# Kernel tuning notes

Measured on AMD Instinct MI355X. Metric: run time of the kernel, lower is better.

Reference implementation:

```python
import jax, jax.numpy as jnp
import numpy as np


def _largest_component_mask(fg):
    # fg: (B,H,W) bool foreground mask. Returns bool mask of the largest
    # 8-connected component per batch element (skimage.measure.label default
    # connectivity for 2D is 8-connectivity).
    B, H, W = fg.shape
    HW = H * W
    big = jnp.int32(HW)  # sentinel label for background / padding
    idx = jnp.arange(HW, dtype=jnp.int32).reshape(1, H, W)
    l0 = jnp.broadcast_to(idx, (B, H, W))

    def neighbor_min(l):
        lm = jnp.where(fg, l, big)
        p = jnp.pad(lm, ((0, 0), (1, 1), (1, 1)), constant_values=HW)
        m = lm
        for di in (-1, 0, 1):
            for dj in (-1, 0, 1):
                if di == 0 and dj == 0:
                    continue
                m = jnp.minimum(m, p[:, 1 + di:1 + di + H, 1 + dj:1 + dj + W])
        return m

    def body(carry):
        l, _ = carry
        # one step of label propagation (min over 8-neighborhood, fg only)
        l2 = jnp.where(fg, jnp.minimum(l, neighbor_min(l)), l)
        # pointer jumping: l <- l[l]  (labels are in-row linear indices)
        lf = l2.reshape(B, HW)
        l2 = jnp.take_along_axis(lf, lf, axis=1).reshape(B, H, W)
        return l2, jnp.any(l2 != l)

    l, _ = jax.lax.while_loop(lambda c: c[1], body, (l0, jnp.bool_(True)))

    lf = l.reshape(B, HW)
    w = fg.reshape(B, HW).astype(jnp.float32)
    counts = jax.vmap(lambda li, wi: jnp.bincount(li, weights=wi, length=HW))(lf, w)
    largest = jnp.argmax(counts, axis=1).astype(jnp.int32)  # (B,) root label of biggest cc
    return (l == largest[:, None, None]) & fg


def setup_inputs() -> dict:
    key = jax.random.key(0)
    x = jax.random.normal(key, (16, 2, 1024, 1024), dtype=jnp.float32)
    return {"x": x}


def reference(x):
    # binary segmentation = argmax over class dim; background class = 0
    binary = jnp.argmax(x, axis=1)          # (B,H,W) int
    fg = binary > 0
    mask = _largest_component_mask(fg)       # (B,H,W) bool, largest cc only
    return x * mask[:, None, :, :].astype(x.dtype)
```

## Files before the change

### kernel.cpp

```cpp
#include <hip/hip_runtime.h>
#include <stdint.h>

static constexpr int BATCH = 16;
static constexpr int Hh = 1024;
static constexpr int Ww = 1024;
static constexpr int HW = Hh * Ww;
static constexpr int NPIX = BATCH * HW;
static constexpr int TS = 64;
static constexpr int TILES_PER_IMG = (Hh / TS) * (Ww / TS);
static constexpr int NODES = TS * 32;

static constexpr int CHUNK = 1024;
static constexpr int NBLK1 = NPIX / CHUNK;
static constexpr int BLK1_PER_B = HW / CHUNK;


__device__ __forceinline__ int find_root_halve(int* parent, int i) {
    while (true) {
        int p = parent[i];
        if (p == i) return i;
        int gp = parent[p];
        if (gp == p) return p;
        parent[i] = gp;
        i = gp;
    }
}

__device__ __forceinline__ int find_root_ro(const int* parent, int i) {
    int p = parent[i];
    while (p != i) { i = p; p = parent[i]; }
    return i;
}

__device__ __forceinline__ void merge_uf(int* parent, int a, int b) {
    while (true) {
        a = find_root_halve(parent, a);
        b = find_root_halve(parent, b);
        if (a == b) return;
        if (a > b) { int t = a; a = b; b = t; }
        int old = atomicMin(&parent[b], a);
        if (old == b) return;
        b = old;
    }
}


__global__ __launch_bounds__(256) void k_local(const float* __restrict__ x,
                                               int* __restrict__ parent,
                                               int* __restrict__ counts,
                                               unsigned long long* __restrict__ best) {
    __shared__ int lab[NODES];
    __shared__ int cnt[NODES];
    __shared__ unsigned char runpos[NODES];
    __shared__ unsigned long long rowmask[TS];

    int tile = blockIdx.x;
    int b = tile >> 8;
    int t = tile & 255;
    int th = t >> 4, tw = t & 15;
    int h0 = th * TS, w0 = tw * TS;
    const float* xb = x + (size_t)b * 2 * (size_t)HW;
    int base = b * HW + h0 * Ww + w0;
    int wv = threadIdx.x >> 6;
    int lane = threadIdx.x & 63;
    unsigned long long below = (lane == 0) ? 0ull : ((1ull << lane) - 1);

    if (tile == 0 && threadIdx.x < BATCH) best[threadIdx.x] = 0ull;

    #pragma unroll
    for (int k = 0; k < NODES / 256; k++) {
        int i = threadIdx.x + k * 256;
        lab[i] = i;
        cnt[i] = 0;
    }

    #pragma unroll
    for (int k = 0; k < TS / 4; k++) {
        int r = (k << 2) | wv;
        int off = (h0 + r) * Ww + w0 + lane;
        float x0 = xb[off];
        float x1 = xb[off + HW];
        bool fg = x1 > x0;
        unsigned long long m = __ballot(fg);
        if (lane == 0) rowmask[r] = m;
        unsigned long long rs = m & ~(m << 1);
        if ((rs >> lane) & 1) {
            int node = (r << 5) | (int)__popcll(rs & below);
            runpos[node] = (unsigned char)lane;
        }
    }
    __syncthreads();

    auto find_lh = [&](int i) {
        while (true) {
            int p = lab[i];
            if (p == i) return i;
            int gp = lab[p];
            if (gp == p) return p;
            lab[i] = gp;
            i = gp;
        }
    };
    auto merge_l = [&](int a, int c) {
        while (true) {
            a = find_lh(a); c = find_lh(c);
            if (a == c) return;
            if (a > c) { int tt = a; a = c; c = tt; }
            int old = atomicMin(&lab[c], a);
            if (old == c) return;
            c = old;
        }
    };

    for (int k = 0; k < TS / 4; k++) {
        int r = (k << 2) | wv;
        if (r == 0) continue;
        unsigned long long m = rowmask[r];
        bool fg = (m >> lane) & 1;
        if (!fg) continue;
        unsigned long long mu = rowmask[r - 1];
        unsigned long long rs = m & ~(m << 1);
        unsigned long long rsu = mu & ~(mu << 1);
        unsigned long long zb = ~m & below;
        int b0 = zb ? (64 - __clzll(zb)) : 0;
        int n0 = (r << 5) | (int)__popcll(rs & ((b0 == 0) ? 0ull : ((1ull << b0) - 1)));
        bool upC = (mu >> lane) & 1;
        bool upL = (lane > 0)  && ((mu >> (lane - 1)) & 1);
        bool upR = (lane < 63) && ((mu >> (lane + 1)) & 1);
        bool atStart = (lane == b0);
        bool atEnd = (lane == 63) || !((m >> (lane + 1)) & 1);
        auto unode = [&](int lu) {
            unsigned long long belu = (lu == 0) ? 0ull : ((1ull << lu) - 1);
            unsigned long long zbu = ~mu & belu;
            int u0 = zbu ? (64 - __clzll(zbu)) : 0;
            return ((r - 1) << 5) | (int)__popcll(rsu & ((u0 == 0) ? 0ull : ((1ull << u0) - 1)));
        };
        if (upC && (atStart || !upL)) merge_l(n0, unode(lane));
        if (atStart && !upC && upL)   merge_l(n0, unode(lane - 1));
        if (atEnd && !upC && upR)     merge_l(n0, unode(lane + 1));
    }
    __syncthreads();

    for (int k = 0; k < TS / 4; k++) {
        int r = (k << 2) | wv;
        unsigned long long m = rowmask[r];
        unsigned long long rs = m & ~(m << 1);
        bool need = (rs >> lane) & 1;
        int root = 0, len = 0;
        if (need) {
            int node = (r << 5) | (int)__popcll(rs & below);
            unsigned long long za = (~m) >> lane;
            len = za ? (int)(__ffsll(za) - 1) : (64 - lane);
            root = node;
            { int q = lab[root]; while (q != root) { root = q; q = lab[root]; } }
            if (root != node) lab[node] = root;
        }
        while (__any(need)) {
            unsigned long long bm = __ballot(need);
            int src = (int)(__ffsll(bm) - 1);
            int rr = __shfl(root, src);
            bool mine = need && (root == rr);
            int v = mine ? len : 0;
            #pragma unroll
            for (int off = 32; off > 0; off >>= 1) v += __shfl_xor(v, off);
            if (lane == src) atomicAdd(&cnt[rr], v);
            if (mine) need = false;
        }
    }
    __syncthreads();

    #pragma unroll
    for (int k = 0; k < TS / 4; k++) {
        int r = (k << 2) | wv;
        unsigned long long m = rowmask[r];
        unsigned long long rs = m & ~(m << 1);
        bool fg = (m >> lane) & 1;
        int g = base + r * Ww + lane;
        int pv = -1, cv = 0;
        if (fg) {
            unsigned long long zb = ~m & below;
            int b0 = zb ? (64 - __clzll(zb)) : 0;
            int node = (r << 5) | (int)__popcll(rs & ((b0 == 0) ? 0ull : ((1ull << b0) - 1)));
            int root = lab[node];
            pv = base + (root >> 5) * Ww + (int)runpos[root];
            if (lane == b0 && root == node) cv = cnt[node];
        }
        parent[g] = pv;
        counts[g] = cv;
    }
}


static constexpr int BORDER_A = (Hh / TS) * Ww;
static constexpr int BORDER_PER_B = BORDER_A + Hh * (Ww / TS) * 2;

__global__ __launch_bounds__(256) void k_border(int* __restrict__ parent) {
    int b = blockIdx.y;
    int t = blockIdx.x * blockDim.x + threadIdx.x;
    int h, w;
    if (t < BORDER_A) {
        h = (t >> 10) << 6;
        w = t & 1023;
    } else {
        int t2 = t - BORDER_A;
        int c = t2 & 31;
        h = t2 >> 5;
        w = ((c >> 1) << 6) + ((c & 1) ? (TS - 1) : 0);
    }
    int i = b * HW + h * Ww + w;
    if (parent[i] < 0) return;
    bool hb = (h & (TS - 1)) == 0;
    bool wb = (w & (TS - 1)) == 0;
    bool we = (w & (TS - 1)) == (TS - 1);
    if (wb && w > 0 && parent[i - 1] >= 0) merge_uf(parent, i, i - 1);
    if (h > 0) {
        if (hb && parent[i - Ww] >= 0) merge_uf(parent, i, i - Ww);
        if ((hb | wb) && w > 0 && parent[i - Ww - 1] >= 0) merge_uf(parent, i, i - Ww - 1);
        if ((hb | we) && w < Ww - 1 && parent[i - Ww + 1] >= 0) merge_uf(parent, i, i - Ww + 1);
    }
}


__global__ __launch_bounds__(256) void k_roots(int* __restrict__ parent,
                                               int* __restrict__ counts) {
    int i = blockIdx.x * blockDim.x + threadIdx.x;
    int c = counts[i];
    if (c <= 0) return;
    int root = find_root_ro(parent, i);
    if (root != i) {
        parent[i] = root;
        atomicAdd(&counts[root], c);
        counts[i] = 0;
    }
}


__global__ __launch_bounds__(256) void k_argmax1(const int* __restrict__ counts,
                                                 unsigned long long* __restrict__ blockmax) {
    int base = blockIdx.x * CHUNK;
    unsigned long long v = 0ull;
    #pragma unroll
    for (int k = 0; k < 4; k++) {
        int i = base + threadIdx.x + k * 256;
        int c = counts[i];
        if (c > 0) {
            unsigned long long o =
                (((unsigned long long)(unsigned)c) << 32) |
                (unsigned long long)(0xFFFFFFFFu - (unsigned)i);
            if (o > v) v = o;
        }
    }
    for (int off = 32; off > 0; off >>= 1) {
        unsigned long long o = __shfl_down(v, off);
        if (o > v) v = o;
    }
    __shared__ unsigned long long sm[4];
    if ((threadIdx.x & 63) == 0) sm[threadIdx.x >> 6] = v;
    __syncthreads();
    if (threadIdx.x == 0) {
        v = sm[0];
        #pragma unroll
        for (int w = 1; w < 4; w++) if (sm[w] > v) v = sm[w];
        blockmax[blockIdx.x] = v;
    }
}


__global__ __launch_bounds__(256) void k_argmax2(const unsigned long long* __restrict__ blockmax,
                                                 unsigned long long* __restrict__ best) {
    int b = blockIdx.x;
    const unsigned long long* src = blockmax + b * BLK1_PER_B;
    unsigned long long v = 0ull;
    #pragma unroll
    for (int k = 0; k < BLK1_PER_B / 256; k++) {
        unsigned long long o = src[threadIdx.x + k * 256];
        if (o > v) v = o;
    }
    for (int off = 32; off > 0; off >>= 1) {
        unsigned long long o = __shfl_down(v, off);
        if (o > v) v = o;
    }
    __shared__ unsigned long long sm[4];
    if ((threadIdx.x & 63) == 0) sm[threadIdx.x >> 6] = v;
    __syncthreads();
    if (threadIdx.x == 0) {
        v = sm[0];
        #pragma unroll
        for (int w = 1; w < 4; w++) if (sm[w] > v) v = sm[w];
        best[b] = v;
    }
}


__global__ __launch_bounds__(256) void k_final(const float* __restrict__ x,
                                               const int* __restrict__ parent,
                                               const unsigned long long* __restrict__ best,
                                               float* __restrict__ out) {
    int i = blockIdx.x * blockDim.x + threadIdx.x;
    int b = i >> 20;
    int p = i & (HW - 1);
    unsigned long long bv = best[b];
    int broot = (int)(0xFFFFFFFFu - (unsigned)(bv & 0xFFFFFFFFull));
    int pr = parent[i];
    int a = (pr >= 0) ? pr : 0;
    int root = parent[a];
    bool mask = (pr >= 0) && (root == broot);
    const float* xb = x + ((size_t)b * 2) * (size_t)HW;
    float* ob = out + ((size_t)b * 2) * (size_t)HW;
    float x0 = xb[p];
    float x1 = xb[p + HW];
    ob[p]      = mask ? x0 : 0.0f;
    ob[p + HW] = mask ? x1 : 0.0f;
}


extern "C" void kernel_launch(void* const* d_in, const int* in_sizes, int n_in,
                              void* d_out, int out_size, void* d_ws, size_t ws_size,
                              hipStream_t stream) {
    const float* x = (const float*)d_in[0];
    float* out = (float*)d_out;

    unsigned long long* best = (unsigned long long*)d_ws;
    int* parent = (int*)((char*)d_ws + 256);
    int* counts = parent + NPIX;
    unsigned long long* blockmax = (unsigned long long*)(counts + NPIX);

    dim3 blk(256);
    dim3 grd(NPIX / 256);
    dim3 grd_tiles(BATCH * TILES_PER_IMG);
    dim3 grd_border(BORDER_PER_B / 256, BATCH);

    k_local   <<<grd_tiles, blk, 0, stream>>>(x, parent, counts, best);
    k_border  <<<grd_border, blk, 0, stream>>>(parent);
    k_roots   <<<grd, blk, 0, stream>>>(parent, counts);
    k_argmax1 <<<dim3(NBLK1), blk, 0, stream>>>(counts, blockmax);
    k_argmax2 <<<dim3(BATCH), blk, 0, stream>>>(blockmax, best);
    k_final   <<<grd, blk, 0, stream>>>(x, parent, best, out);
}
```

Measured before the change: 602.3 us.

## Compact component roots into per-image list instead of dense count scans

```diff
diff --git a/kernel.cpp b/kernel.cpp
--- a/kernel.cpp
+++ b/kernel.cpp
@@ -10,9 +10,8 @@
 static constexpr int TILES_PER_IMG = (Hh / TS) * (Ww / TS);
 static constexpr int NODES = TS * 32;
 
-static constexpr int CHUNK = 1024;
-static constexpr int NBLK1 = NPIX / CHUNK;
-static constexpr int BLK1_PER_B = HW / CHUNK;
+static constexpr int CAPB = 65536;
+static constexpr int NB1  = CAPB / 1024;
 
 
 __device__ __forceinline__ int find_root_halve(int* parent, int i) {
@@ -48,11 +47,14 @@
 __global__ __launch_bounds__(256) void k_local(const float* __restrict__ x,
                                                int* __restrict__ parent,
                                                int* __restrict__ counts,
-                                               unsigned long long* __restrict__ best) {
+                                               unsigned long long* __restrict__ list,
+                                               unsigned* __restrict__ nlist) {
     __shared__ int lab[NODES];
     __shared__ int cnt[NODES];
     __shared__ unsigned char runpos[NODES];
     __shared__ unsigned long long rowmask[TS];
+    __shared__ int wbase[4];
+    __shared__ int blkbase;
 
     int tile = blockIdx.x;
     int b = tile >> 8;
@@ -64,8 +66,6 @@
     int wv = threadIdx.x >> 6;
     int lane = threadIdx.x & 63;
     unsigned long long below = (lane == 0) ? 0ull : ((1ull << lane) - 1);
-
-    if (tile == 0 && threadIdx.x < BATCH) best[threadIdx.x] = 0ull;
 
     #pragma unroll
     for (int k = 0; k < NODES / 256; k++) {
@@ -176,17 +176,52 @@
         unsigned long long rs = m & ~(m << 1);
         bool fg = (m >> lane) & 1;
         int g = base + r * Ww + lane;
-        int pv = -1, cv = 0;
+        int pv = -1;
         if (fg) {
             unsigned long long zb = ~m & below;
             int b0 = zb ? (64 - __clzll(zb)) : 0;
             int node = (r << 5) | (int)__popcll(rs & ((b0 == 0) ? 0ull : ((1ull << b0) - 1)));
             int root = lab[node];
             pv = base + (root >> 5) * Ww + (int)runpos[root];
-            if (lane == b0 && root == node) cv = cnt[node];
         }
         parent[g] = pv;
-        counts[g] = cv;
+    }
+
+    int wtot = 0;
+    unsigned rootbits = 0;
+    #pragma unroll
+    for (int k = 0; k < NODES / 256; k++) {
+        int node = (k << 8) | threadIdx.x;
+        bool isr = cnt[node] > 0;
+        if (isr) rootbits |= (1u << k);
+        unsigned long long bm = __ballot(isr);
+        wtot += (int)__popcll(bm);
+    }
+    if (lane == 0) wbase[wv] = wtot;
+    __syncthreads();
+    if (threadIdx.x == 0) {
+        int s0 = wbase[0], s1 = wbase[1], s2 = wbase[2], s3 = wbase[3];
+        blkbase = (int)atomicAdd(&nlist[b << 5], (unsigned)(s0 + s1 + s2 + s3));
+        wbase[0] = 0; wbase[1] = s0; wbase[2] = s0 + s1; wbase[3] = s0 + s1 + s2;
+    }
+    __syncthreads();
+    int woff = blkbase + wbase[wv];
+    #pragma unroll
+    for (int k = 0; k < NODES / 256; k++) {
+        bool isr = (rootbits >> k) & 1;
+        unsigned long long bm = __ballot(isr);
+        if (isr) {
+            int slot = woff + (int)__popcll(bm & below);
+            if (slot < CAPB) {
+                int node = (k << 8) | threadIdx.x;
+                int g = base + (node >> 5) * Ww + (int)runpos[node];
+                list[(size_t)b * CAPB + slot] =
+                    (((unsigned long long)(unsigned)cnt[node]) << 32) |
+                    (unsigned long long)(0xFFFFFFFFu - (unsigned)g);
+                counts[g] = 0;
+            }
+        }
+        woff += (int)__popcll(bm);
     }
 }
 
@@ -222,31 +257,54 @@
 
 
 __global__ __launch_bounds__(256) void k_roots(int* __restrict__ parent,
-                                               int* __restrict__ counts) {
-    int i = blockIdx.x * blockDim.x + threadIdx.x;
-    int c = counts[i];
-    if (c <= 0) return;
-    int root = find_root_ro(parent, i);
-    if (root != i) {
-        parent[i] = root;
-        atomicAdd(&counts[root], c);
-        counts[i] = 0;
-    }
-}
-
-
-__global__ __launch_bounds__(256) void k_argmax1(const int* __restrict__ counts,
+                                               int* __restrict__ counts,
+                                               unsigned long long* __restrict__ list,
+                                               const unsigned* __restrict__ nlist) {
+    int b = blockIdx.y;
+    int n = (int)nlist[b << 5]; if (n > CAPB) n = CAPB;
+    int j = blockIdx.x * 256 + threadIdx.x;
+    bool need = j < n;
+    int r = 0, c = 0;
+    size_t idx = (size_t)b * CAPB + j;
+    if (need) {
+        unsigned long long e = list[idx];
+        int g = (int)(0xFFFFFFFFu - (unsigned)(e & 0xFFFFFFFFull));
+        c = (int)(e >> 32);
+        r = find_root_ro(parent, g);
+        if (r != g) parent[g] = r;
+        list[idx] = (unsigned long long)(0xFFFFFFFFu - (unsigned)r);
+    }
+    int lane = threadIdx.x & 63;
+    while (__any(need)) {
+        unsigned long long bm = __ballot(need);
+        int src = (int)(__ffsll(bm) - 1);
+        int rr = __shfl(r, src);
+        bool mine = need && (r == rr);
+        int v = mine ? c : 0;
+        #pragma unroll
+        for (int off = 32; off > 0; off >>= 1) v += __shfl_xor(v, off);
+        if (lane == src) atomicAdd(&counts[rr], v);
+        if (mine) need = false;
+    }
+}
+
+
+__global__ __launch_bounds__(256) void k_argmax1(const unsigned long long* __restrict__ list,
+                                                 const int* __restrict__ counts,
+                                                 const unsigned* __restrict__ nlist,
                                                  unsigned long long* __restrict__ blockmax) {
-    int base = blockIdx.x * CHUNK;
+    int b = blockIdx.y;
+    int n = (int)nlist[b << 5]; if (n > CAPB) n = CAPB;
     unsigned long long v = 0ull;
     #pragma unroll
     for (int k = 0; k < 4; k++) {
-        int i = base + threadIdx.x + k * 256;
-        int c = counts[i];
-        if (c > 0) {
+        int j = blockIdx.x * 1024 + k * 256 + threadIdx.x;
+        if (j < n) {
+            unsigned rinv = (unsigned)(list[(size_t)b * CAPB + j] & 0xFFFFFFFFull);
+            int r = (int)(0xFFFFFFFFu - rinv);
+            int c = counts[r];
             unsigned long long o =
-                (((unsigned long long)(unsigned)c) << 32) |
-                (unsigned long long)(0xFFFFFFFFu - (unsigned)i);
+                (((unsigned long long)(unsigned)c) << 32) | (unsigned long long)rinv;
             if (o > v) v = o;
         }
     }
@@ -261,7 +319,7 @@
         v = sm[0];
         #pragma unroll
         for (int w = 1; w < 4; w++) if (sm[w] > v) v = sm[w];
-        blockmax[blockIdx.x] = v;
+        blockmax[b * NB1 + blockIdx.x] = v;
     }
 }
 
@@ -269,13 +327,8 @@
 __global__ __launch_bounds__(256) void k_argmax2(const unsigned long long* __restrict__ blockmax,
                                                  unsigned long long* __restrict__ best) {
     int b = blockIdx.x;
-    const unsigned long long* src = blockmax + b * BLK1_PER_B;
     unsigned long long v = 0ull;
-    #pragma unroll
-    for (int k = 0; k < BLK1_PER_B / 256; k++) {
-        unsigned long long o = src[threadIdx.x + k * 256];
-        if (o > v) v = o;
-    }
+    if (threadIdx.x < NB1) v = blockmax[b * NB1 + threadIdx.x];
     for (int off = 32; off > 0; off >>= 1) {
         unsigned long long o = __shfl_down(v, off);
         if (o > v) v = o;
@@ -321,19 +374,25 @@
     float* out = (float*)d_out;
 
     unsigned long long* best = (unsigned long long*)d_ws;
-    int* parent = (int*)((char*)d_ws + 256);
+    unsigned* nlist = (unsigned*)((char*)d_ws + 256);
+    int* parent = (int*)((char*)d_ws + 4096);
     int* counts = parent + NPIX;
     unsigned long long* blockmax = (unsigned long long*)(counts + NPIX);
+    unsigned long long* list = blockmax + 1024;
 
     dim3 blk(256);
     dim3 grd(NPIX / 256);
     dim3 grd_tiles(BATCH * TILES_PER_IMG);
     dim3 grd_border(BORDER_PER_B / 256, BATCH);
-
-    k_local   <<<grd_tiles, blk, 0, stream>>>(x, parent, counts, best);
+    dim3 grd_roots(CAPB / 256, BATCH);
+    dim3 grd_arg1(NB1, BATCH);
+
+    hipMemsetAsync(nlist, 0, 2048, stream);
+
+    k_local   <<<grd_tiles, blk, 0, stream>>>(x, parent, counts, list, nlist);
     k_border  <<<grd_border, blk, 0, stream>>>(parent);
-    k_roots   <<<grd, blk, 0, stream>>>(parent, counts);
-    k_argmax1 <<<dim3(NBLK1), blk, 0, stream>>>(counts, blockmax);
+    k_roots   <<<grd_roots, blk, 0, stream>>>(parent, counts, list, nlist);
+    k_argmax1 <<<grd_arg1, blk, 0, stream>>>(list, counts, nlist, blockmax);
     k_argmax2 <<<dim3(BATCH), blk, 0, stream>>>(blockmax, best);
     k_final   <<<grd, blk, 0, stream>>>(x, parent, best, out);
 }
```

Result: faster. 555.4 us (-7.8%).
